# Performance work log

Hardware: AMD Instinct MI355X
Metric: run time of the kernel (lower is better)

Reference implementation:

```python
import jax, jax.numpy as jnp
import numpy as np
import math

EPS = 1e-8
LN_EPS = 1e-5
B, S, E, NH = 2, 2048, 1024, 4
DH = E // NH


def setup_inputs() -> dict:
    key = jax.random.key(0)
    ks = jax.random.split(key, 7)
    std_g = math.sqrt(2.0 / (5.0 * 3 * E))
    return {
        "q": jax.random.normal(ks[0], (B, S, E), dtype=jnp.float32),
        "k": jax.random.normal(ks[1], (B, S, E), dtype=jnp.float32),
        "v": jax.random.normal(ks[2], (B, S, E), dtype=jnp.float32),
        "igate_w": jax.random.normal(ks[3], (NH, 3 * E), dtype=jnp.float32) * std_g,
        "igate_b": jax.random.normal(ks[4], (NH,), dtype=jnp.float32) * 0.1,
        "fgate_w": jax.random.normal(ks[5], (NH, 3 * E), dtype=jnp.float32) * std_g,
        "fgate_b": jnp.linspace(3.4, 6.0, NH, dtype=jnp.float32),
        "out_w": jnp.zeros((E,), dtype=jnp.float32),  # residual affine weight (scale = 1 + out_w)
    }


def _mlstm_cell(q, k, v, igate_w, igate_b, fgate_w, fgate_b, out_w):
    Bq, Sq, Eq = q.shape
    # gate pre-activations from concatenated q,k,v: [B,S,NH]
    if_in = jnp.concatenate([q, k, v], axis=-1)
    ig = jnp.einsum("bsf,hf->bsh", if_in, igate_w) + igate_b
    fg = jnp.einsum("bsf,hf->bsh", if_in, fgate_w) + fgate_b
    ig = jnp.transpose(ig, (0, 2, 1))[..., None]  # [B,NH,S,1]
    fg = jnp.transpose(fg, (0, 2, 1))[..., None]  # [B,NH,S,1]

    # split heads: [B,NH,S,DH]
    qh = q.reshape(Bq, Sq, NH, DH).transpose(0, 2, 1, 3)
    kh = k.reshape(Bq, Sq, NH, DH).transpose(0, 2, 1, 3)
    vh = v.reshape(Bq, Sq, NH, DH).transpose(0, 2, 1, 3)

    # cumulative log forget gates -> causal decay matrix (log space)
    log_fg = jax.nn.log_sigmoid(fg)                           # [B,NH,S,1]
    cs = jnp.cumsum(log_fg, axis=2)                           # [B,NH,S,1]
    cs_shift = jnp.concatenate([jnp.zeros_like(cs[:, :, :1]), cs[:, :, :-1]], axis=2)
    # log_fg_matrix[i,j] = cumsum[i] - cumsum[j-1], masked causal
    logfg_mat = cs - jnp.swapaxes(cs_shift, -2, -1)           # [B,NH,S,S]
    ltr = jnp.tril(jnp.ones((Sq, Sq), dtype=bool))
    logfg_mat = jnp.where(ltr, logfg_mat, -jnp.inf)
    log_D = logfg_mat + jnp.swapaxes(ig, -2, -1)              # + igate row broadcast [B,NH,1,S]

    max_log_D = jnp.max(log_D, axis=-1, keepdims=True)        # [B,NH,S,1]
    D = jnp.exp(log_D - max_log_D)                            # stabilized decay matrix

    qk = jnp.einsum("bhsd,bhtd->bhst", qh, kh / math.sqrt(DH))
    C = qk * D
    sum_C_abs = jnp.abs(jnp.sum(C, axis=-1, keepdims=True))
    normaliser = jnp.maximum(sum_C_abs, jnp.exp(-max_log_D))  # robust normalizer
    C_norm = C / (normaliser + EPS)
    h = jnp.einsum("bhst,bhtd->bhsd", C_norm, vh)             # [B,NH,S,DH]

    # MultiHeadLayerNorm == group_norm with NH groups, per-channel residual weight
    mean = jnp.mean(h, axis=-1, keepdims=True)
    var = jnp.mean((h - mean) ** 2, axis=-1, keepdims=True)
    h_norm = (h - mean) / jnp.sqrt(var + LN_EPS)
    scale = (1.0 + out_w).reshape(1, NH, 1, DH)
    h_norm = h_norm * scale

    return h_norm.transpose(0, 2, 1, 3).reshape(Bq, Sq, Eq)


def reference(q, k, v, igate_w, igate_b, fgate_w, fgate_b, out_w):
    return _mlstm_cell(q, k, v, igate_w, igate_b, fgate_w, fgate_b, out_w)
```

## Files before the change

kernel.cpp:

```cpp
#include <hip/hip_runtime.h>
#include <hip/hip_bf16.h>
#include <math.h>

#define Bb  2
#define Ss  2048
#define Ee  1024
#define NHh 4
#define DHh 256
#define BH  (Bb*NHh)
#define TI  64
#define TIB 128
#define TJ  32
#define NT2 (Ss/TI)
#define NTB (Ss/TIB)
#define NJT (Ss/TJ)

typedef short        s8v   __attribute__((ext_vector_type(8)));
typedef float        f4v   __attribute__((ext_vector_type(4)));
typedef float        f16v  __attribute__((ext_vector_type(16)));
typedef unsigned int u4v   __attribute__((ext_vector_type(4)));
typedef unsigned int u2v   __attribute__((ext_vector_type(2)));

__device__ inline unsigned pkbf2(float a, float b) {
    __hip_bfloat162 h2 = __float22bfloat162_rn(float2{a, b});
    unsigned u;
    __builtin_memcpy(&u, &h2, 4);
    return u;
}

__device__ inline void async16(const void* g, void* l) {
    __builtin_amdgcn_global_load_lds(
        (const __attribute__((address_space(1))) void*)g,
        (__attribute__((address_space(3))) void*)l, 16, 0, 0);
}

__global__ __launch_bounds__(256) void gates_prep_kernel(
    const float* __restrict__ q, const float* __restrict__ k, const float* __restrict__ v,
    const float* __restrict__ igw, const float* __restrict__ igb,
    const float* __restrict__ fgw, const float* __restrict__ fgb,
    float* __restrict__ ig_out, float* __restrict__ fg_out,
    unsigned short* __restrict__ Kimg, unsigned short* __restrict__ Vimg)
{
    int bidx = blockIdx.x;
    int tid = threadIdx.x;

    if (bidx >= 512) {
        int pidx = bidx - 512;
        int bh = pidx >> 6, jt = pidx & 63;
        int b = bh >> 2, h = bh & 3;
        int J0 = jt * TJ;
        const size_t hoff = (size_t)h * DHh;
        unsigned short* Kt = Kimg + (size_t)pidx * 1024 * 8;
        unsigned short* Vt = Vimg + (size_t)pidx * 1024 * 8;

        {
            int kR = tid >> 3, kc0 = tid & 7;
            const float* src = k + ((size_t)(b * Ss + J0 + kR)) * Ee + hoff;
#pragma unroll
            for (int p = 0; p < 4; p++) {
                int cc = kc0 + 8 * p;
                float4 x0 = ((const float4*)(src + cc * 8))[0];
                float4 x1 = ((const float4*)(src + cc * 8))[1];
                u4v wv;
                wv.x = pkbf2(x0.x, x0.y); wv.y = pkbf2(x0.z, x0.w);
                wv.z = pkbf2(x1.x, x1.y); wv.w = pkbf2(x1.z, x1.w);
                *(u4v*)&Kt[(kR * 32 + (cc ^ (kR & 7))) * 8] = wv;
            }
        }
        {
            int vdp = tid & 127, vjb = tid >> 7;
            int d0 = vdp * 2;
#pragma unroll
            for (int p = 0; p < 2; p++) {
                int jc = vjb + 2 * p;
                const float* vbase = v + ((size_t)(b * Ss + J0 + jc * 8)) * Ee + hoff + d0;
                float2 e0 = *(const float2*)(vbase);
                float2 e1 = *(const float2*)(vbase + Ee);
                float2 e2 = *(const float2*)(vbase + 2 * Ee);
                float2 e3 = *(const float2*)(vbase + 3 * Ee);
                float2 e4 = *(const float2*)(vbase + 4 * Ee);
                float2 e5 = *(const float2*)(vbase + 5 * Ee);
                float2 e6 = *(const float2*)(vbase + 6 * Ee);
                float2 e7 = *(const float2*)(vbase + 7 * Ee);
                int swz = jc ^ (vdp & 3);
                u4v w0, w1;
                w0.x = pkbf2(e0.x, e1.x); w0.y = pkbf2(e2.x, e3.x);
                w0.z = pkbf2(e4.x, e5.x); w0.w = pkbf2(e6.x, e7.x);
                w1.x = pkbf2(e0.y, e1.y); w1.y = pkbf2(e2.y, e3.y);
                w1.z = pkbf2(e4.y, e5.y); w1.w = pkbf2(e6.y, e7.y);
                *(u4v*)&Vt[(d0 * 4 + swz) * 8] = w0;
                *(u4v*)&Vt[((d0 + 1) * 4 + swz) * 8] = w1;
            }
        }
        return;
    }

    int sc = bidx >> 1, hp = bidx & 1;
    __shared__ float wl[4][3072];
    __shared__ float pw[4][8];

#pragma unroll
    for (int c = 0; c < 4; c++) {
        int h = hp * 2 + (c >> 1);
        const float* src = ((c & 1) ? fgw : igw) + (size_t)h * 3 * Ee;
        for (int idx = tid * 4; idx < 3 * Ee; idx += 1024)
            *(float4*)&wl[c][idx] = *(const float4*)(src + idx);
    }
    __syncthreads();

    int c4 = tid * 4;
    int w = tid >> 6, lane = tid & 63;

    for (int sp = 0; sp < 8; sp++) {
        int bs0 = sc * 16 + sp * 2;
        float4 qa = *(const float4*)(q + (size_t)bs0 * Ee + c4);
        float4 ka = *(const float4*)(k + (size_t)bs0 * Ee + c4);
        float4 va = *(const float4*)(v + (size_t)bs0 * Ee + c4);
        float4 qb = *(const float4*)(q + (size_t)(bs0 + 1) * Ee + c4);
        float4 kb = *(const float4*)(k + (size_t)(bs0 + 1) * Ee + c4);
        float4 vb = *(const float4*)(v + (size_t)(bs0 + 1) * Ee + c4);
        float red[8];
#pragma unroll
        for (int c = 0; c < 4; c++) {
            const float* wc = wl[c];
            float4 wq = *(const float4*)&wc[c4];
            float4 wk = *(const float4*)&wc[Ee + c4];
            float4 wv = *(const float4*)&wc[2 * Ee + c4];
            float x0 = qa.x*wq.x + qa.y*wq.y + qa.z*wq.z + qa.w*wq.w
                     + ka.x*wk.x + ka.y*wk.y + ka.z*wk.z + ka.w*wk.w
                     + va.x*wv.x + va.y*wv.y + va.z*wv.z + va.w*wv.w;
            float x1 = qb.x*wq.x + qb.y*wq.y + qb.z*wq.z + qb.w*wq.w
                     + kb.x*wk.x + kb.y*wk.y + kb.z*wk.z + kb.w*wk.w
                     + vb.x*wv.x + vb.y*wv.y + vb.z*wv.z + vb.w*wv.w;
            for (int off = 32; off > 0; off >>= 1) {
                x0 += __shfl_down(x0, off, 64);
                x1 += __shfl_down(x1, off, 64);
            }
            red[c] = x0; red[4 + c] = x1;
        }
        __syncthreads();
        if (lane == 0) {
#pragma unroll
            for (int c = 0; c < 8; c++) pw[w][c] = red[c];
        }
        __syncthreads();
        if (tid < 8) {
            float t = pw[0][tid] + pw[1][tid] + pw[2][tid] + pw[3][tid];
            int rr = tid >> 2, cc = tid & 3;
            int h = hp * 2 + (cc >> 1);
            int bs = bs0 + rr;
            int b = bs >> 11, s = bs & 2047;
            size_t o = ((size_t)(b * NHh + h)) * Ss + s;
            if (cc & 1) fg_out[o] = t + fgb[h];
            else        ig_out[o] = t + igb[h];
        }
    }
}

#define CHUNK 8
__global__ __launch_bounds__(256) void scan_kernel(
    const float* __restrict__ ig, const float* __restrict__ fg,
    float* __restrict__ a_out, float* __restrict__ M_out, float* __restrict__ nf_out)
{
    int bh = blockIdx.x;
    int tid = threadIdx.x;
    const float* igp = ig + (size_t)bh * Ss;
    const float* fgp = fg + (size_t)bh * Ss;
    int s0 = tid * CHUNK;

    float ls[CHUNK], cs[CHUNK];
    float tot = 0.f;
#pragma unroll
    for (int c = 0; c < CHUNK; c++) {
        float x = fgp[s0 + c];
        float l = fminf(x, 0.f) - log1pf(expf(-fabsf(x)));
        ls[c] = l; tot += l; cs[c] = tot;
    }
    __shared__ float sc[256];
    sc[tid] = tot; __syncthreads();
    for (int off = 1; off < 256; off <<= 1) {
        float add = (tid >= off) ? sc[tid - off] : 0.f;
        __syncthreads();
        sc[tid] += add;
        __syncthreads();
    }
    float excl = sc[tid] - tot;

    float av[CHUNK], pmax[CHUNK];
    float tmax = -INFINITY;
#pragma unroll
    for (int c = 0; c < CHUNK; c++) {
        float csf  = excl + cs[c];
        float csm1 = csf - ls[c];
        float a = igp[s0 + c] - csm1;
        av[c] = a;
        tmax = fmaxf(tmax, a);
        pmax[c] = tmax;
        cs[c] = csf;
    }
    __shared__ float sm[256];
    sm[tid] = tmax; __syncthreads();
    for (int off = 1; off < 256; off <<= 1) {
        float other = (tid >= off) ? sm[tid - off] : -INFINITY;
        __syncthreads();
        sm[tid] = fmaxf(sm[tid], other);
        __syncthreads();
    }
    float emax = (tid > 0) ? sm[tid - 1] : -INFINITY;
#pragma unroll
    for (int c = 0; c < CHUNK; c++) {
        float M = fmaxf(emax, pmax[c]);
        size_t o = (size_t)bh * Ss + s0 + c;
        a_out[o]  = av[c];
        M_out[o]  = M;
        nf_out[o] = expf(-cs[c] - M);
    }
}

__global__ __launch_bounds__(256, 2) void mlstm_big2(
    const float* __restrict__ qp,
    const unsigned short* __restrict__ Kimg, const unsigned short* __restrict__ Vimg,
    const float* __restrict__ a_ws, const float* __restrict__ M_ws,
    float* __restrict__ outF, float* __restrict__ Hpart, float* __restrict__ rsbuf)
{
    int bidx = blockIdx.x;
    int qd = bidx >> 7, u = bidx & 127;
    int bh = u & 7;
    int r  = u >> 3;
    int T  = (qd < 2) ? (15 - r) : r;
    int sg = qd;
    int b = bh >> 2, h = bh & 3;
    int I0 = T * TIB;
    int tid = threadIdx.x;

    const int tot = 4 * T + 4;
    const int jt_beg = (sg * tot) / 4;
    const int jt_end = ((sg + 1) * tot) / 4;
    const size_t hoff = (size_t)h * DHh;
    float* Hdst = (sg == 0) ? outF : (Hpart + (size_t)(sg - 1) * Bb * Ss * Ee);

    if (jt_beg >= jt_end) {
        float4 z = {0.f, 0.f, 0.f, 0.f};
        for (int t = tid; t < TIB * 64; t += 256) {
            int r2 = t >> 6, c = t & 63;
            *(float4*)(Hdst + ((size_t)(b * Ss + I0 + r2)) * Ee + hoff + 4 * c) = z;
        }
        if (tid < TIB) rsbuf[(size_t)sg * BH * Ss + (size_t)bh * Ss + I0 + tid] = 0.f;
        return;
    }

    __shared__ unsigned short KF[2][1024 * 8];
    __shared__ unsigned short VF[2][1024 * 8];
    __shared__ unsigned short PF[512 * 8];
    __shared__ float a_s[2][TJ];
    __shared__ float rs_s[TIB];

    const int iq   = tid >> 6;
    const int lane = tid & 63;
    const int lm = lane & 15, q4 = lane >> 4;

    s8v qf0[8], qf1[8];
    {
        const float* qrow0 = qp + ((size_t)(b * Ss + I0 + iq * 16 + lm)) * Ee + hoff;
        const float* qrow1 = qrow0 + (size_t)64 * Ee;
#pragma unroll
        for (int ks = 0; ks < 8; ks++) {
            const float4* p0 = (const float4*)(qrow0 + ks * 32 + q4 * 8);
            float4 x0 = p0[0], x1 = p0[1];
            union { s8v v; unsigned u[4]; } rr;
            rr.u[0] = pkbf2(x0.x, x0.y);
            rr.u[1] = pkbf2(x0.z, x0.w);
            rr.u[2] = pkbf2(x1.x, x1.y);
            rr.u[3] = pkbf2(x1.z, x1.w);
            qf0[ks] = rr.v;
            const float4* p1 = (const float4*)(qrow1 + ks * 32 + q4 * 8);
            float4 y0 = p1[0], y1 = p1[1];
            union { s8v v; unsigned u[4]; } ss;
            ss.u[0] = pkbf2(y0.x, y0.y);
            ss.u[1] = pkbf2(y0.z, y0.w);
            ss.u[2] = pkbf2(y1.x, y1.y);
            ss.u[3] = pkbf2(y1.z, y1.w);
            qf1[ks] = ss.v;
        }
    }
    const int  i_row0 = I0 + iq * 16 + lm;
    const int  i_row1 = i_row0 + 64;
    const float Mi0 = M_ws[(size_t)bh * Ss + i_row0];
    const float Mi1 = M_ws[(size_t)bh * Ss + i_row1];

    f4v acc0[16], acc1[16];
#pragma unroll
    for (int t = 0; t < 16; t++) {
        acc0[t][0]=0.f; acc0[t][1]=0.f; acc0[t][2]=0.f; acc0[t][3]=0.f;
        acc1[t][0]=0.f; acc1[t][1]=0.f; acc1[t][2]=0.f; acc1[t][3]=0.f;
    }
    float rs_a0 = 0.f, rs_a1 = 0.f;
    const float inv_sqrt_dh = 0.0625f;

    const unsigned short* Kb = Kimg + (size_t)(bh * NJT) * 1024 * 8;
    const unsigned short* Vb = Vimg + (size_t)(bh * NJT) * 1024 * 8;

    {
        const unsigned short* Kt = Kb + (size_t)jt_beg * 1024 * 8;
        const unsigned short* Vt = Vb + (size_t)jt_beg * 1024 * 8;
#pragma unroll
        for (int p = 0; p < 4; p++) {
            int cbase = (iq * 4 + p) * 64;
            async16(Kt + (size_t)(cbase + lane) * 8, &KF[0][cbase * 8]);
            async16(Vt + (size_t)(cbase + lane) * 8, &VF[0][cbase * 8]);
        }
        if (tid < TJ) a_s[0][tid] = a_ws[(size_t)bh * Ss + jt_beg * TJ + tid];
    }

    int cur = 0;
    for (int jt = jt_beg; jt < jt_end; jt++, cur ^= 1) {
        __syncthreads();

        if (jt + 1 < jt_end) {
            const unsigned short* Kt = Kb + (size_t)(jt + 1) * 1024 * 8;
            const unsigned short* Vt = Vb + (size_t)(jt + 1) * 1024 * 8;
#pragma unroll
            for (int p = 0; p < 4; p++) {
                int cbase = (iq * 4 + p) * 64;
                async16(Kt + (size_t)(cbase + lane) * 8, &KF[cur ^ 1][cbase * 8]);
                async16(Vt + (size_t)(cbase + lane) * 8, &VF[cur ^ 1][cbase * 8]);
            }
            if (tid < TJ) a_s[cur ^ 1][tid] = a_ws[(size_t)bh * Ss + (jt + 1) * TJ + tid];
        }
        const int J0 = jt * TJ;

        f4v c00 = {0.f,0.f,0.f,0.f}, c01 = c00, c10 = c00, c11 = c00;
#pragma unroll
        for (int ks = 0; ks < 8; ks++) {
            int swzk = ((ks * 4 + q4) ^ (lm & 7)) * 8;
            s8v af0 = *(const s8v*)&KF[cur][(lm * 32) * 8 + swzk];
            s8v af1 = *(const s8v*)&KF[cur][((16 + lm) * 32) * 8 + swzk];
            c00 = __builtin_amdgcn_mfma_f32_16x16x32_bf16(af0, qf0[ks], c00, 0, 0, 0);
            c01 = __builtin_amdgcn_mfma_f32_16x16x32_bf16(af1, qf0[ks], c01, 0, 0, 0);
            c10 = __builtin_amdgcn_mfma_f32_16x16x32_bf16(af0, qf1[ks], c10, 0, 0, 0);
            c11 = __builtin_amdgcn_mfma_f32_16x16x32_bf16(af1, qf1[ks], c11, 0, 0, 0);
        }
        {
            float rsum0 = 0.f, rsum1 = 0.f;
#pragma unroll
            for (int t = 0; t < 2; t++) {
                const f4v ca = t ? c01 : c00;
                const f4v cb = t ? c11 : c10;
                const int jb = t * 16 + q4 * 4;
                float p0[4], p1[4];
#pragma unroll
                for (int rr = 0; rr < 4; rr++) {
                    int jg = J0 + jb + rr;
                    float ev = __expf(a_s[cur][jb + rr] - Mi0) * inv_sqrt_dh;
                    float ev1 = __expf(a_s[cur][jb + rr] - Mi1) * inv_sqrt_dh;
                    float pv0 = 0.f, pv1 = 0.f;
                    if (jg <= i_row0) pv0 = ca[rr] * ev;
                    if (jg <= i_row1) pv1 = cb[rr] * ev1;
                    p0[rr] = pv0; rsum0 += pv0;
                    p1[rr] = pv1; rsum1 += pv1;
                }
                int kb = t * 2 + (q4 >> 1);
                int cidx = (iq * 64 + lm * 4 + (kb ^ (lm & 3))) * 8 + (q4 & 1) * 4;
                u2v pw0, pw1;
                pw0.x = pkbf2(p0[0], p0[1]); pw0.y = pkbf2(p0[2], p0[3]);
                pw1.x = pkbf2(p1[0], p1[1]); pw1.y = pkbf2(p1[2], p1[3]);
                *(u2v*)&PF[cidx]            = pw0;
                *(u2v*)&PF[256 * 8 + cidx]  = pw1;
            }
            rsum0 += __shfl_xor(rsum0, 16);
            rsum0 += __shfl_xor(rsum0, 32);
            rs_a0 += rsum0;
            rsum1 += __shfl_xor(rsum1, 16);
            rsum1 += __shfl_xor(rsum1, 32);
            rs_a1 += rsum1;
        }
        int pidx = (iq * 64 + lm * 4 + (q4 ^ (lm & 3))) * 8;
        s8v pa0 = *(const s8v*)&PF[pidx];
        s8v pa1 = *(const s8v*)&PF[256 * 8 + pidx];

#pragma unroll
        for (int db = 0; db < 16; db++) {
            int d = db * 16 + lm;
            s8v vb = *(const s8v*)&VF[cur][(d * 4 + (q4 ^ ((d >> 1) & 3))) * 8];
            acc0[db] = __builtin_amdgcn_mfma_f32_16x16x32_bf16(pa0, vb, acc0[db], 0, 0, 0);
            acc1[db] = __builtin_amdgcn_mfma_f32_16x16x32_bf16(pa1, vb, acc1[db], 0, 0, 0);
        }
    }

    if (q4 == 0) {
        rs_s[iq * 16 + lm] = rs_a0;
        rs_s[64 + iq * 16 + lm] = rs_a1;
    }
    __syncthreads();
    if (tid < TIB)
        rsbuf[(size_t)sg * BH * Ss + (size_t)bh * Ss + I0 + tid] = rs_s[tid];

#pragma unroll
    for (int rr = 0; rr < 4; rr++) {
        float* row0 = Hdst + ((size_t)(b * Ss + I0 + iq * 16 + q4 * 4 + rr)) * Ee + hoff + lm;
        float* row1 = row0 + (size_t)64 * Ee;
#pragma unroll
        for (int db = 0; db < 16; db++) {
            row0[db * 16] = acc0[db][rr];
            row1[db * 16] = acc1[db][rr];
        }
    }
}

template<int PARTS>
__global__ __launch_bounds__(256, 4) void mlstm_fallback(
    const float* __restrict__ qp, const float* __restrict__ kp, const float* __restrict__ vp,
    const float* __restrict__ a_ws, const float* __restrict__ M_ws,
    float* __restrict__ outF, float* __restrict__ Hpart, float* __restrict__ rsbuf)
{
    int bidx = blockIdx.x;
    int bh, T, sg;
    if (PARTS == 1) {
        bh = bidx & 7; T = (NT2 - 1) - (bidx >> 3); sg = 0;
    } else {
        int qd = bidx >> 8, u = bidx & 255;
        bh = u & 7;
        int r = u >> 3;
        T  = qd ? r : (31 - r);
        sg = r & 1;
    }
    int b = bh >> 2, h = bh & 3;
    int I0 = T * TI;
    int tid = threadIdx.x;

    const int tot = 2 * T + 2;
    const int jt_beg = (sg * tot) / PARTS;
    const int jt_end = ((sg + 1) * tot) / PARTS;
    const size_t hoff = (size_t)h * DHh;
    float* Hdst = (sg == 0) ? outF : (Hpart + (size_t)(sg - 1) * Bb * Ss * Ee);

    if (jt_beg >= jt_end) {
        float4 z = {0.f, 0.f, 0.f, 0.f};
        for (int t = tid; t < TI * 64; t += 256) {
            int r2 = t >> 6, c = t & 63;
            *(float4*)(Hdst + ((size_t)(b * Ss + I0 + r2)) * Ee + hoff + 4 * c) = z;
        }
        if (tid < TI) rsbuf[(size_t)sg * BH * Ss + (size_t)bh * Ss + I0 + tid] = 0.f;
        return;
    }

    __shared__ unsigned short KF[1024 * 8];
    __shared__ unsigned short VF[1024 * 8];
    __shared__ unsigned short PF[256 * 8];
    __shared__ float a_s[TJ];
    __shared__ float rs_s[TI];

    const int iq   = tid >> 6;
    const int lane = tid & 63;
    const int lm = lane & 15, q4 = lane >> 4;
    const int m5 = lane & 31, hl = lane >> 5;

    s8v qf[8];
    {
        const float* qrow = qp + ((size_t)(b * Ss + I0 + iq * 16 + lm)) * Ee + hoff;
#pragma unroll
        for (int ks = 0; ks < 8; ks++) {
            const float4* p = (const float4*)(qrow + ks * 32 + q4 * 8);
            float4 x0 = p[0], x1 = p[1];
            union { s8v v; unsigned u[4]; } rr;
            rr.u[0] = pkbf2(x0.x, x0.y);
            rr.u[1] = pkbf2(x0.z, x0.w);
            rr.u[2] = pkbf2(x1.x, x1.y);
            rr.u[3] = pkbf2(x1.z, x1.w);
            qf[ks] = rr.v;
        }
    }
    const int  i_row = I0 + iq * 16 + lm;
    const float Mi = M_ws[(size_t)bh * Ss + i_row];

    f16v acc[4];
#pragma unroll
    for (int t = 0; t < 4; t++)
#pragma unroll
        for (int i = 0; i < 16; i++) acc[t][i] = 0.f;
    float rs_acc = 0.f;

    const float inv_sqrt_dh = 0.0625f;
    const int kR  = tid >> 3, kc0 = tid & 7;
    const int vdp = tid & 127, vjb = tid >> 7;

    for (int jt = jt_beg; jt < jt_end; jt++) {
        const int J0 = jt * TJ;
        __syncthreads();
        {
            const float* src = kp + ((size_t)(b * Ss + J0 + kR)) * Ee + hoff;
#pragma unroll
            for (int p = 0; p < 4; p++) {
                int cc = kc0 + 8 * p;
                float4 x0 = ((const float4*)(src + cc * 8))[0];
                float4 x1 = ((const float4*)(src + cc * 8))[1];
                u4v wv;
                wv.x = pkbf2(x0.x, x0.y); wv.y = pkbf2(x0.z, x0.w);
                wv.z = pkbf2(x1.x, x1.y); wv.w = pkbf2(x1.z, x1.w);
                *(u4v*)&KF[(kR * 32 + (cc ^ (kR & 7))) * 8] = wv;
            }
            int d0 = vdp * 2;
#pragma unroll
            for (int p = 0; p < 2; p++) {
                int jc = vjb + 2 * p;
                const float* vbase = vp + ((size_t)(b * Ss + J0 + jc * 8)) * Ee + hoff + d0;
                float2 e0 = *(const float2*)(vbase);
                float2 e1 = *(const float2*)(vbase + Ee);
                float2 e2 = *(const float2*)(vbase + 2 * Ee);
                float2 e3 = *(const float2*)(vbase + 3 * Ee);
                float2 e4 = *(const float2*)(vbase + 4 * Ee);
                float2 e5 = *(const float2*)(vbase + 5 * Ee);
                float2 e6 = *(const float2*)(vbase + 6 * Ee);
                float2 e7 = *(const float2*)(vbase + 7 * Ee);
                int swz = jc ^ (vdp & 3);
                u4v w0, w1;
                w0.x = pkbf2(e0.x, e1.x); w0.y = pkbf2(e2.x, e3.x);
                w0.z = pkbf2(e4.x, e5.x); w0.w = pkbf2(e6.x, e7.x);
                w1.x = pkbf2(e0.y, e1.y); w1.y = pkbf2(e2.y, e3.y);
                w1.z = pkbf2(e4.y, e5.y); w1.w = pkbf2(e6.y, e7.y);
                *(u4v*)&VF[(d0 * 4 + swz) * 8] = w0;
                *(u4v*)&VF[((d0 + 1) * 4 + swz) * 8] = w1;
            }
        }
        if (tid < TJ) a_s[tid] = a_ws[(size_t)bh * Ss + J0 + tid];
        __syncthreads();

        f4v c0 = {0.f, 0.f, 0.f, 0.f}, c1 = c0;
#pragma unroll
        for (int ks = 0; ks < 8; ks++) {
            int swzk = ((ks * 4 + q4) ^ (lm & 7)) * 8;
            s8v af0 = *(const s8v*)&KF[(lm * 32) * 8 + swzk];
            s8v af1 = *(const s8v*)&KF[((16 + lm) * 32) * 8 + swzk];
            c0 = __builtin_amdgcn_mfma_f32_16x16x32_bf16(af0, qf[ks], c0, 0, 0, 0);
            c1 = __builtin_amdgcn_mfma_f32_16x16x32_bf16(af1, qf[ks], c1, 0, 0, 0);
        }
        {
            float rsum = 0.f;
#pragma unroll
            for (int t = 0; t < 2; t++) {
                const f4v cc = t ? c1 : c0;
                const int jb = t * 16 + q4 * 4;
                float p[4];
#pragma unroll
                for (int rr = 0; rr < 4; rr++) {
                    int jg = J0 + jb + rr;
                    float pv = 0.f;
                    if (jg <= i_row) pv = cc[rr] * inv_sqrt_dh * __expf(a_s[jb + rr] - Mi);
                    p[rr] = pv; rsum += pv;
                }
                u2v pwv;
                pwv.x = pkbf2(p[0], p[1]);
                pwv.y = pkbf2(p[2], p[3]);
                int i = iq * 16 + lm;
                int kb = t * 2 + (q4 >> 1);
                *(u2v*)&PF[(i * 4 + (kb ^ ((i >> 1) & 3))) * 8 + (q4 & 1) * 4] = pwv;
            }
            rsum += __shfl_xor(rsum, 16);
            rsum += __shfl_xor(rsum, 32);
            rs_acc += rsum;
        }
        __syncthreads();

#pragma unroll
        for (int ks2 = 0; ks2 < 2; ks2++) {
            int swz2 = ((ks2 * 2 + hl) ^ ((m5 >> 1) & 3)) * 8;
            s8v pa0 = *(const s8v*)&PF[(m5 * 4) * 8 + swz2];
            s8v pa1 = *(const s8v*)&PF[((32 + m5) * 4) * 8 + swz2];
            s8v vb0 = *(const s8v*)&VF[((iq * 32 + m5) * 4) * 8 + swz2];
            s8v vb1 = *(const s8v*)&VF[(((iq + 4) * 32 + m5) * 4) * 8 + swz2];
            acc[0] = __builtin_amdgcn_mfma_f32_32x32x16_bf16(pa0, vb0, acc[0], 0, 0, 0);
            acc[1] = __builtin_amdgcn_mfma_f32_32x32x16_bf16(pa0, vb1, acc[1], 0, 0, 0);
            acc[2] = __builtin_amdgcn_mfma_f32_32x32x16_bf16(pa1, vb0, acc[2], 0, 0, 0);
            acc[3] = __builtin_amdgcn_mfma_f32_32x32x16_bf16(pa1, vb1, acc[3], 0, 0, 0);
        }
    }

    if (q4 == 0) rs_s[iq * 16 + lm] = rs_acc;
    __syncthreads();
    if (tid < TI)
        rsbuf[(size_t)sg * BH * Ss + (size_t)bh * Ss + I0 + tid] = rs_s[tid];

#pragma unroll
    for (int im = 0; im < 2; im++)
#pragma unroll
        for (int ns = 0; ns < 2; ns++) {
            const f16v av = acc[im * 2 + ns];
            const int col = (iq + 4 * ns) * 32 + m5;
#pragma unroll
            for (int rr = 0; rr < 16; rr++) {
                int row = I0 + im * 32 + (rr & 3) + 8 * (rr >> 2) + 4 * hl;
                Hdst[((size_t)(b * Ss + row)) * Ee + hoff + col] = av[rr];
            }
        }
}

template<int PARTS>
__global__ __launch_bounds__(256) void combine_kernel(
    const float* __restrict__ Hb, const float* __restrict__ rsbuf,
    const float* __restrict__ nf_ws, const float* __restrict__ out_w,
    float* __restrict__ outF)
{
    int rid = blockIdx.x * 4 + (threadIdx.x >> 6);
    int lane = threadIdx.x & 63;
    int bh = rid >> 11, s = rid & 2047;
    int b = bh >> 2, h = bh & 3;
    size_t base = ((size_t)(b * Ss + s)) * Ee + (size_t)h * DHh + lane * 4;
    float4 ha = *(const float4*)(outF + base);
    float rs = rsbuf[(size_t)bh * Ss + s];
#pragma unroll
    for (int k = 1; k < PARTS; k++) {
        float4 hb = *(const float4*)(Hb + (size_t)(k - 1) * Bb * Ss * Ee + base);
        ha.x += hb.x; ha.y += hb.y; ha.z += hb.z; ha.w += hb.w;
        rs += rsbuf[(size_t)k * BH * Ss + (size_t)bh * Ss + s];
    }
    float nfv = nf_ws[(size_t)bh * Ss + s];
    float invn = 1.f / (fmaxf(fabsf(rs), nfv) + 1e-8f);
    float4 x;
    x.x = ha.x * invn; x.y = ha.y * invn; x.z = ha.z * invn; x.w = ha.w * invn;
    float sx = x.x + x.y + x.z + x.w;
    float sq = x.x*x.x + x.y*x.y + x.z*x.z + x.w*x.w;
#pragma unroll
    for (int off = 1; off < 64; off <<= 1) {
        sx += __shfl_xor(sx, off);
        sq += __shfl_xor(sq, off);
    }
    float mean = sx * (1.f / DHh);
    float var  = sq * (1.f / DHh) - mean * mean;
    float rstd = rsqrtf(var + 1e-5f);
    float4 w4 = *(const float4*)(out_w + (size_t)h * DHh + lane * 4);
    float4 o;
    o.x = (x.x - mean) * rstd * (1.f + w4.x);
    o.y = (x.y - mean) * rstd * (1.f + w4.y);
    o.z = (x.z - mean) * rstd * (1.f + w4.z);
    o.w = (x.w - mean) * rstd * (1.f + w4.w);
    *(float4*)(outF + base) = o;
}

extern "C" void kernel_launch(void* const* d_in, const int* in_sizes, int n_in,
                              void* d_out, int out_size, void* d_ws, size_t ws_size,
                              hipStream_t stream) {
    const float* q   = (const float*)d_in[0];
    const float* k   = (const float*)d_in[1];
    const float* v   = (const float*)d_in[2];
    const float* igw = (const float*)d_in[3];
    const float* igb = (const float*)d_in[4];
    const float* fgw = (const float*)d_in[5];
    const float* fgb = (const float*)d_in[6];
    const float* ow  = (const float*)d_in[7];
    float* out = (float*)d_out;

    float* ws = (float*)d_ws;
    float* ig = ws;
    float* fg = ws + 16384;
    float* aa = ws + 32768;
    float* MM = ws + 49152;
    float* nf = ws + 65536;
    float* rsb = ws + 81920;
    const size_t base_f = 81920 + 65536;
    unsigned short* KimgP = (unsigned short*)(ws + base_f);
    const size_t img_u = (size_t)BH * NJT * 1024 * 8;
    unsigned short* VimgP = KimgP + img_u;
    float* HpartImg = (float*)(VimgP + img_u);
    float* HpartRaw = ws + base_f;
    const size_t HP = (size_t)Bb * Ss * Ee;

    const size_t need4  = base_f * 4 + 2 * img_u * 2 + 3 * HP * 4;
    const size_t need2  = base_f * 4 + 1 * HP * 4;

    if (ws_size >= need4) {
        gates_prep_kernel<<<1024, 256, 0, stream>>>(q, k, v, igw, igb, fgw, fgb,
                                                    ig, fg, KimgP, VimgP);
        scan_kernel<<<BH, 256, 0, stream>>>(ig, fg, aa, MM, nf);
        mlstm_big2<<<512, 256, 0, stream>>>(q, KimgP, VimgP, aa, MM,
                                            out, HpartImg, rsb);
        combine_kernel<4><<<BH * Ss / 4, 256, 0, stream>>>(HpartImg, rsb, nf, ow, out);
    } else if (ws_size >= need2) {
        gates_prep_kernel<<<512, 256, 0, stream>>>(q, k, v, igw, igb, fgw, fgb,
                                                   ig, fg, nullptr, nullptr);
        scan_kernel<<<BH, 256, 0, stream>>>(ig, fg, aa, MM, nf);
        mlstm_fallback<2><<<512, 256, 0, stream>>>(q, k, v, aa, MM, out, HpartRaw, rsb);
        combine_kernel<2><<<BH * Ss / 4, 256, 0, stream>>>(HpartRaw, rsb, nf, ow, out);
    } else {
        gates_prep_kernel<<<512, 256, 0, stream>>>(q, k, v, igw, igb, fgw, fgb,
                                                   ig, fg, nullptr, nullptr);
        scan_kernel<<<BH, 256, 0, stream>>>(ig, fg, aa, MM, nf);
        mlstm_fallback<1><<<256, 256, 0, stream>>>(q, k, v, aa, MM, out, HpartRaw, rsb);
        combine_kernel<1><<<BH * Ss / 4, 256, 0, stream>>>(HpartRaw, rsb, nf, ow, out);
    }
}
```

Before: 199.0 us.

## Balance causal attention work by pairing row tiles across equal-size blocks

Adds a new main kernel that pairs a short row tile with its mirrored long tile and splits their combined key-tile range evenly across 8 blocks per pair. Each block handles about the same number of key tiles, which removes the load imbalance of the old fixed 4-way split. A matching combine kernel sums a variable number of partial outputs per row tile. The zero-fill early exit in the old kernel is removed. The new path needs a larger workspace (seven partial output buffers and a bigger rsbuf) and is only taken when that much is available.

```diff
diff --git a/kernel.cpp b/kernel.cpp
--- a/kernel.cpp
+++ b/kernel.cpp
@@ -217,6 +217,208 @@
     }
 }
 
+__global__ __launch_bounds__(256, 2) void mlstm_eq(
+    const float* __restrict__ qp,
+    const unsigned short* __restrict__ Kimg, const unsigned short* __restrict__ Vimg,
+    const float* __restrict__ a_ws, const float* __restrict__ M_ws,
+    float* __restrict__ outF, float* __restrict__ Hpart, float* __restrict__ rsbuf)
+{
+    int bidx = blockIdx.x;
+    int bh = bidx & 7;
+    int w  = bidx >> 3;
+    int pr = w >> 3;
+    int c8 = w & 7;
+    int b = bh >> 2, h = bh & 3;
+    int tid = threadIdx.x;
+
+    const int nA = 4 * pr + 4;
+    const int s0 = (c8 * 68) >> 3;
+    const int e0 = ((c8 + 1) * 68) >> 3;
+    int qA = 0;
+#pragma unroll
+    for (int cc = 0; cc < 8; cc++)
+        if ((((cc + 1) * 68) >> 3) <= nA) qA++;
+
+    const size_t hoff = (size_t)h * DHh;
+    const size_t HP = (size_t)Bb * Ss * Ee;
+
+    __shared__ unsigned short KF[2][1024 * 8];
+    __shared__ unsigned short VF[2][1024 * 8];
+    __shared__ unsigned short PF[512 * 8];
+    __shared__ float a_s[2][TJ];
+    __shared__ float rs_s[TIB];
+
+    const int iq   = tid >> 6;
+    const int lane = tid & 63;
+    const int lm = lane & 15, q4 = lane >> 4;
+    const float inv_sqrt_dh = 0.0625f;
+
+    const unsigned short* Kb = Kimg + (size_t)(bh * NJT) * 1024 * 8;
+    const unsigned short* Vb = Vimg + (size_t)(bh * NJT) * 1024 * 8;
+    const float* a_base = a_ws + (size_t)bh * Ss;
+
+    for (int pc = 0; pc < 2; pc++) {
+        int T, jt_beg, jt_end, ord;
+        if (pc == 0) {
+            if (s0 >= nA) continue;
+            T = pr; jt_beg = s0;
+            jt_end = (e0 < nA) ? e0 : nA;
+            ord = c8;
+        } else {
+            if (e0 <= nA) continue;
+            T = 15 - pr;
+            jt_beg = (s0 > nA ? s0 : nA) - nA;
+            jt_end = e0 - nA;
+            ord = c8 - qA;
+        }
+        const int I0 = T * TIB;
+        float* Hdst = (ord == 0) ? outF : (Hpart + (size_t)(ord - 1) * HP);
+
+        s8v qf0[8], qf1[8];
+        {
+            const float* qrow0 = qp + ((size_t)(b * Ss + I0 + iq * 16 + lm)) * Ee + hoff;
+            const float* qrow1 = qrow0 + (size_t)64 * Ee;
+#pragma unroll
+            for (int ks = 0; ks < 8; ks++) {
+                const float4* p0 = (const float4*)(qrow0 + ks * 32 + q4 * 8);
+                float4 x0 = p0[0], x1 = p0[1];
+                union { s8v v; unsigned u[4]; } rr;
+                rr.u[0] = pkbf2(x0.x, x0.y);
+                rr.u[1] = pkbf2(x0.z, x0.w);
+                rr.u[2] = pkbf2(x1.x, x1.y);
+                rr.u[3] = pkbf2(x1.z, x1.w);
+                qf0[ks] = rr.v;
+                const float4* p1 = (const float4*)(qrow1 + ks * 32 + q4 * 8);
+                float4 y0 = p1[0], y1 = p1[1];
+                union { s8v v; unsigned u[4]; } ss;
+                ss.u[0] = pkbf2(y0.x, y0.y);
+                ss.u[1] = pkbf2(y0.z, y0.w);
+                ss.u[2] = pkbf2(y1.x, y1.y);
+                ss.u[3] = pkbf2(y1.z, y1.w);
+                qf1[ks] = ss.v;
+            }
+        }
+        const int  i_row0 = I0 + iq * 16 + lm;
+        const int  i_row1 = i_row0 + 64;
+        const float Mi0 = M_ws[(size_t)bh * Ss + i_row0];
+        const float Mi1 = M_ws[(size_t)bh * Ss + i_row1];
+
+        f4v acc0[16], acc1[16];
+#pragma unroll
+        for (int t = 0; t < 16; t++) {
+            acc0[t][0]=0.f; acc0[t][1]=0.f; acc0[t][2]=0.f; acc0[t][3]=0.f;
+            acc1[t][0]=0.f; acc1[t][1]=0.f; acc1[t][2]=0.f; acc1[t][3]=0.f;
+        }
+        float rs_a0 = 0.f, rs_a1 = 0.f;
+
+        {
+            const unsigned short* Kt = Kb + (size_t)jt_beg * 1024 * 8;
+            const unsigned short* Vt = Vb + (size_t)jt_beg * 1024 * 8;
+#pragma unroll
+            for (int p = 0; p < 4; p++) {
+                int cbase = (iq * 4 + p) * 64;
+                async16(Kt + (size_t)(cbase + lane) * 8, &KF[0][cbase * 8]);
+                async16(Vt + (size_t)(cbase + lane) * 8, &VF[0][cbase * 8]);
+            }
+            if (tid < TJ) a_s[0][tid] = a_base[jt_beg * TJ + tid];
+        }
+
+        int cur = 0;
+        for (int jt = jt_beg; jt < jt_end; jt++, cur ^= 1) {
+            __syncthreads();
+
+            if (jt + 1 < jt_end) {
+                const unsigned short* Kt = Kb + (size_t)(jt + 1) * 1024 * 8;
+                const unsigned short* Vt = Vb + (size_t)(jt + 1) * 1024 * 8;
+#pragma unroll
+                for (int p = 0; p < 4; p++) {
+                    int cbase = (iq * 4 + p) * 64;
+                    async16(Kt + (size_t)(cbase + lane) * 8, &KF[cur ^ 1][cbase * 8]);
+                    async16(Vt + (size_t)(cbase + lane) * 8, &VF[cur ^ 1][cbase * 8]);
+                }
+                if (tid < TJ) a_s[cur ^ 1][tid] = a_base[(jt + 1) * TJ + tid];
+            }
+            const int J0 = jt * TJ;
+
+            f4v c00 = {0.f,0.f,0.f,0.f}, c01 = c00, c10 = c00, c11 = c00;
+#pragma unroll
+            for (int ks = 0; ks < 8; ks++) {
+                int swzk = ((ks * 4 + q4) ^ (lm & 7)) * 8;
+                s8v af0 = *(const s8v*)&KF[cur][(lm * 32) * 8 + swzk];
+                s8v af1 = *(const s8v*)&KF[cur][((16 + lm) * 32) * 8 + swzk];
+                c00 = __builtin_amdgcn_mfma_f32_16x16x32_bf16(af0, qf0[ks], c00, 0, 0, 0);
+                c01 = __builtin_amdgcn_mfma_f32_16x16x32_bf16(af1, qf0[ks], c01, 0, 0, 0);
+                c10 = __builtin_amdgcn_mfma_f32_16x16x32_bf16(af0, qf1[ks], c10, 0, 0, 0);
+                c11 = __builtin_amdgcn_mfma_f32_16x16x32_bf16(af1, qf1[ks], c11, 0, 0, 0);
+            }
+            {
+                float rsum0 = 0.f, rsum1 = 0.f;
+#pragma unroll
+                for (int t = 0; t < 2; t++) {
+                    const f4v ca = t ? c01 : c00;
+                    const f4v cb = t ? c11 : c10;
+                    const int jb = t * 16 + q4 * 4;
+                    float p0[4], p1[4];
+#pragma unroll
+                    for (int rr = 0; rr < 4; rr++) {
+                        int jg = J0 + jb + rr;
+                        float ev = __expf(a_s[cur][jb + rr] - Mi0) * inv_sqrt_dh;
+                        float ev1 = __expf(a_s[cur][jb + rr] - Mi1) * inv_sqrt_dh;
+                        float pv0 = 0.f, pv1 = 0.f;
+                        if (jg <= i_row0) pv0 = ca[rr] * ev;
+                        if (jg <= i_row1) pv1 = cb[rr] * ev1;
+                        p0[rr] = pv0; rsum0 += pv0;
+                        p1[rr] = pv1; rsum1 += pv1;
+                    }
+                    int kb = t * 2 + (q4 >> 1);
+                    int cidx = (iq * 64 + lm * 4 + (kb ^ (lm & 3))) * 8 + (q4 & 1) * 4;
+                    u2v pw0, pw1;
+                    pw0.x = pkbf2(p0[0], p0[1]); pw0.y = pkbf2(p0[2], p0[3]);
+                    pw1.x = pkbf2(p1[0], p1[1]); pw1.y = pkbf2(p1[2], p1[3]);
+                    *(u2v*)&PF[cidx]            = pw0;
+                    *(u2v*)&PF[256 * 8 + cidx]  = pw1;
+                }
+                rsum0 += __shfl_xor(rsum0, 16);
+                rsum0 += __shfl_xor(rsum0, 32);
+                rs_a0 += rsum0;
+                rsum1 += __shfl_xor(rsum1, 16);
+                rsum1 += __shfl_xor(rsum1, 32);
+                rs_a1 += rsum1;
+            }
+            int pidx = (iq * 64 + lm * 4 + (q4 ^ (lm & 3))) * 8;
+            s8v pa0 = *(const s8v*)&PF[pidx];
+            s8v pa1 = *(const s8v*)&PF[256 * 8 + pidx];
+
+#pragma unroll
+            for (int db = 0; db < 16; db++) {
+                int d = db * 16 + lm;
+                s8v vb = *(const s8v*)&VF[cur][(d * 4 + (q4 ^ ((d >> 1) & 3))) * 8];
+                acc0[db] = __builtin_amdgcn_mfma_f32_16x16x32_bf16(pa0, vb, acc0[db], 0, 0, 0);
+                acc1[db] = __builtin_amdgcn_mfma_f32_16x16x32_bf16(pa1, vb, acc1[db], 0, 0, 0);
+            }
+        }
+
+        if (q4 == 0) {
+            rs_s[iq * 16 + lm] = rs_a0;
+            rs_s[64 + iq * 16 + lm] = rs_a1;
+        }
+        __syncthreads();
+        if (tid < TIB)
+            rsbuf[(size_t)ord * BH * Ss + (size_t)bh * Ss + I0 + tid] = rs_s[tid];
+
+#pragma unroll
+        for (int rr = 0; rr < 4; rr++) {
+            float* row0 = Hdst + ((size_t)(b * Ss + I0 + iq * 16 + q4 * 4 + rr)) * Ee + hoff + lm;
+            float* row1 = row0 + (size_t)64 * Ee;
+#pragma unroll
+            for (int db = 0; db < 16; db++) {
+                row0[db * 16] = acc0[db][rr];
+                row1[db * 16] = acc1[db][rr];
+            }
+        }
+    }
+}
+
 __global__ __launch_bounds__(256, 2) void mlstm_big2(
     const float* __restrict__ qp,
     const unsigned short* __restrict__ Kimg, const unsigned short* __restrict__ Vimg,
@@ -238,16 +440,6 @@
     const int jt_end = ((sg + 1) * tot) / 4;
     const size_t hoff = (size_t)h * DHh;
     float* Hdst = (sg == 0) ? outF : (Hpart + (size_t)(sg - 1) * Bb * Ss * Ee);
-
-    if (jt_beg >= jt_end) {
-        float4 z = {0.f, 0.f, 0.f, 0.f};
-        for (int t = tid; t < TIB * 64; t += 256) {
-            int r2 = t >> 6, c = t & 63;
-            *(float4*)(Hdst + ((size_t)(b * Ss + I0 + r2)) * Ee + hoff + 4 * c) = z;
-        }
-        if (tid < TIB) rsbuf[(size_t)sg * BH * Ss + (size_t)bh * Ss + I0 + tid] = 0.f;
-        return;
-    }
 
     __shared__ unsigned short KF[2][1024 * 8];
     __shared__ unsigned short VF[2][1024 * 8];
@@ -594,6 +786,64 @@
         }
 }
 
+__global__ __launch_bounds__(256) void combine_var(
+    const float* __restrict__ Hb, const float* __restrict__ rsbuf,
+    const float* __restrict__ nf_ws, const float* __restrict__ out_w,
+    float* __restrict__ outF)
+{
+    int rid = blockIdx.x * 4 + (threadIdx.x >> 6);
+    int lane = threadIdx.x & 63;
+    int bh = rid >> 11, s = rid & 2047;
+    int b = bh >> 2, h = bh & 3;
+    int T = s >> 7;
+    int p;
+    if (T <= 7) {
+        int nA = 4 * T + 4;
+        p = 0;
+#pragma unroll
+        for (int cc = 0; cc < 8; cc++)
+            if (((cc * 68) >> 3) < nA) p++;
+    } else {
+        int nA = 64 - 4 * T;
+        int q = 0;
+#pragma unroll
+        for (int cc = 0; cc < 8; cc++)
+            if ((((cc + 1) * 68) >> 3) <= nA) q++;
+        p = 8 - q;
+    }
+
+    size_t base = ((size_t)(b * Ss + s)) * Ee + (size_t)h * DHh + lane * 4;
+    const size_t HP = (size_t)Bb * Ss * Ee;
+    float4 ha = *(const float4*)(outF + base);
+    float rs = rsbuf[(size_t)bh * Ss + s];
+    for (int k = 1; k < p; k++) {
+        float4 hb = *(const float4*)(Hb + (size_t)(k - 1) * HP + base);
+        ha.x += hb.x; ha.y += hb.y; ha.z += hb.z; ha.w += hb.w;
+        rs += rsbuf[(size_t)k * BH * Ss + (size_t)bh * Ss + s];
+    }
+    float nfv = nf_ws[(size_t)bh * Ss + s];
+    float invn = 1.f / (fmaxf(fabsf(rs), nfv) + 1e-8f);
+    float4 x;
+    x.x = ha.x * invn; x.y = ha.y * invn; x.z = ha.z * invn; x.w = ha.w * invn;
+    float sx = x.x + x.y + x.z + x.w;
+    float sq = x.x*x.x + x.y*x.y + x.z*x.z + x.w*x.w;
+#pragma unroll
+    for (int off = 1; off < 64; off <<= 1) {
+        sx += __shfl_xor(sx, off);
+        sq += __shfl_xor(sq, off);
+    }
+    float mean = sx * (1.f / DHh);
+    float var  = sq * (1.f / DHh) - mean * mean;
+    float rstd = rsqrtf(var + 1e-5f);
+    float4 w4 = *(const float4*)(out_w + (size_t)h * DHh + lane * 4);
+    float4 o;
+    o.x = (x.x - mean) * rstd * (1.f + w4.x);
+    o.y = (x.y - mean) * rstd * (1.f + w4.y);
+    o.z = (x.z - mean) * rstd * (1.f + w4.z);
+    o.w = (x.w - mean) * rstd * (1.f + w4.w);
+    *(float4*)(outF + base) = o;
+}
+
 template<int PARTS>
 __global__ __launch_bounds__(256) void combine_kernel(
     const float* __restrict__ Hb, const float* __restrict__ rsbuf,
@@ -656,7 +906,7 @@
     float* MM = ws + 49152;
     float* nf = ws + 65536;
     float* rsb = ws + 81920;
-    const size_t base_f = 81920 + 65536;
+    const size_t base_f = 81920 + 131072;
     unsigned short* KimgP = (unsigned short*)(ws + base_f);
     const size_t img_u = (size_t)BH * NJT * 1024 * 8;
     unsigned short* VimgP = KimgP + img_u;
@@ -664,10 +914,18 @@
     float* HpartRaw = ws + base_f;
     const size_t HP = (size_t)Bb * Ss * Ee;
 
-    const size_t need4  = base_f * 4 + 2 * img_u * 2 + 3 * HP * 4;
-    const size_t need2  = base_f * 4 + 1 * HP * 4;
-
-    if (ws_size >= need4) {
+    const size_t need_eq = base_f * 4 + 2 * img_u * 2 + 7 * HP * 4;
+    const size_t need4   = base_f * 4 + 2 * img_u * 2 + 3 * HP * 4;
+    const size_t need2   = base_f * 4 + 1 * HP * 4;
+
+    if (ws_size >= need_eq) {
+        gates_prep_kernel<<<1024, 256, 0, stream>>>(q, k, v, igw, igb, fgw, fgb,
+                                                    ig, fg, KimgP, VimgP);
+        scan_kernel<<<BH, 256, 0, stream>>>(ig, fg, aa, MM, nf);
+        mlstm_eq<<<512, 256, 0, stream>>>(q, KimgP, VimgP, aa, MM,
+                                          out, HpartImg, rsb);
+        combine_var<<<BH * Ss / 4, 256, 0, stream>>>(HpartImg, rsb, nf, ow, out);
+    } else if (ws_size >= need4) {
         gates_prep_kernel<<<1024, 256, 0, stream>>>(q, k, v, igw, igb, fgw, fgb,
                                                     ig, fg, KimgP, VimgP);
         scan_kernel<<<BH, 256, 0, stream>>>(ig, fg, aa, MM, nf);
```

Result: slower. 218.2 us (+9.6%).
